# Kernel optimization log

Hardware: AMD Instinct MI355X
Metric: run time of the kernel (lower is better)

Reference implementation:

```python
import jax, jax.numpy as jnp
import numpy as np

WIDTH = 32
DEPTH = 3
B, J, K = 16, 256, 384
C_MODEL, C_OBS, C_META = 1, 1, 6
C_IN = C_MODEL + C_OBS + C_META  # concat channels fed to image_mlp


def _mlp(h, W_stack, b_stack):
    # depth x (Linear -> ReLU) hidden blocks
    for d in range(W_stack.shape[0]):
        h = jax.nn.relu(h @ W_stack[d] + b_stack[d])
    return h


def setup_inputs() -> dict:
    key = jax.random.key(0)
    ks = jax.random.split(key, 14)
    Imodel = jax.random.normal(ks[0], (B, J, K, C_MODEL), jnp.float32)
    Iobs = jax.random.normal(ks[1], (B, J, K, C_OBS), jnp.float32)
    metadata = jax.random.normal(ks[2], (B, J, K, C_META), jnp.float32)
    mask = jax.random.randint(ks[3], (B, J, K, 1), 0, 2) > 0

    def init_w(k, fan_in, fan_out):
        return jax.random.normal(k, (fan_in, fan_out), jnp.float32) / np.sqrt(fan_in)

    params = dict(
        W_img_in=init_w(ks[4], C_IN, WIDTH),
        b_img_in=jnp.zeros((WIDTH,), jnp.float32),
        W_img=jax.random.normal(ks[5], (DEPTH, WIDTH, WIDTH), jnp.float32) / np.sqrt(WIDTH),
        b_img=jnp.zeros((DEPTH, WIDTH), jnp.float32),
        W_lin_in=init_w(ks[6], C_META, WIDTH),
        b_lin_in=jnp.zeros((WIDTH,), jnp.float32),
        W_mlp=jax.random.normal(ks[7], (DEPTH, WIDTH, WIDTH), jnp.float32) / np.sqrt(WIDTH),
        b_mlp=jnp.zeros((DEPTH, WIDTH), jnp.float32),
        W_out=init_w(ks[8], WIDTH, 1),
        b_out=jnp.zeros((1,), jnp.float32),
    )
    return dict(Imodel=Imodel, Iobs=Iobs, metadata=metadata, mask=mask,
                sample_size=32, **params)


def reference(Imodel, Iobs, metadata, mask, sample_size,
              W_img_in, b_img_in, W_img, b_img,
              W_lin_in, b_lin_in, W_mlp, b_mlp, W_out, b_out):
    batch = Iobs.shape[0]
    # p: probability of each image having any observed reflection, normalized
    p = jnp.any(mask, axis=-2)[..., 0].astype(jnp.float32)  # [B, J]
    p = p / jnp.sum(p, axis=-1, keepdims=True)
    # multinomial without replacement via Gumbel top-k (fixed key)
    g = jax.random.gumbel(jax.random.key(42), p.shape, jnp.float32)
    scores = jnp.log(p) + g  # -inf where p == 0, never selected
    _, j = jax.lax.top_k(scores, sample_size)  # [B, S]
    idx = j[:, :, None, None]  # broadcast over K and channel dims

    im = jnp.take_along_axis(Imodel, idx, axis=1)    # [B, S, K, 1]
    io = jnp.take_along_axis(Iobs, idx, axis=1)      # [B, S, K, 1]
    md = jnp.take_along_axis(metadata, idx, axis=1)  # [B, S, K, 6]
    image_data = jnp.concatenate((im, io, md), axis=-1)  # [B, S, K, 8]
    image_mask = jnp.take_along_axis(mask, idx, axis=1).astype(jnp.float32)  # [B, S, K, 1]

    # image_mlp: input linear + depth hidden blocks
    h = image_data @ W_img_in + b_img_in
    h = _mlp(h, W_img, b_img)  # [B, S, K, WIDTH]
    # masked mean over sampled reflections
    image_rep = jnp.sum(image_mask * h, axis=(1, 2), keepdims=True)
    image_rep = image_rep / jnp.sum(image_mask, axis=(1, 2), keepdims=True)  # [B,1,1,WIDTH]

    scale = metadata @ W_lin_in + b_lin_in  # [B, J, K, WIDTH]
    scale = scale + image_rep
    scale = _mlp(scale, W_mlp, b_mlp)
    scale = scale @ W_out + b_out  # [B, J, K, 1]
    return jnp.where(mask, scale, 0.0)
```

## Files before the change

### kernel.cpp

```cpp
#include <hip/hip_runtime.h>
#include <hip/hip_bf16.h>
#include <stdint.h>

#define BB   16
#define JJ   256
#define KK   384
#define NROW (BB * JJ)
#define NPOS ((size_t)BB * JJ * KK)

#define WS_FLAG  0
#define WS_SEL   64
#define WS_VINT  2176
#define WS_VBYTE (WS_VINT + NROW * 4)
#define WS_PART  (WS_VBYTE + NROW * 4)
#define WS_REPB  (WS_PART + 512 * 33 * 4)

typedef float f32x4 __attribute__((ext_vector_type(4)));
typedef short bf16x8 __attribute__((ext_vector_type(8)));

__device__ __forceinline__ uint32_t rotl32(uint32_t x, int r) {
  return (x << r) | (x >> (32 - r));
}

__device__ __forceinline__ void threefry2x32_k42(uint32_t c0, uint32_t c1,
                                                 uint32_t& o0, uint32_t& o1) {
  const uint32_t ks0 = 0u, ks1 = 42u, ks2 = 0x1BD11BDAu ^ 0u ^ 42u;
  uint32_t x0 = c0 + ks0, x1 = c1 + ks1;
#define TFR(r) { x0 += x1; x1 = rotl32(x1, r); x1 ^= x0; }
  TFR(13) TFR(15) TFR(26) TFR(6)   x0 += ks1; x1 += ks2 + 1u;
  TFR(17) TFR(29) TFR(16) TFR(24)  x0 += ks2; x1 += ks0 + 2u;
  TFR(13) TFR(15) TFR(26) TFR(6)   x0 += ks0; x1 += ks1 + 3u;
  TFR(17) TFR(29) TFR(16) TFR(24)  x0 += ks1; x1 += ks2 + 4u;
  TFR(13) TFR(15) TFR(26) TFR(6)   x0 += ks2; x1 += ks0 + 5u;
#undef TFR
  o0 = x0; o1 = x1;
}

__device__ __forceinline__ uint32_t jax_bits(uint32_t t) {
  uint32_t o0, o1;
  threefry2x32_k42(0u, t, o0, o1);
  return o0 ^ o1;
}

__device__ __forceinline__ void split2(float x, short& h, short& l) {
  const unsigned short hu = __builtin_bit_cast(unsigned short, __float2bfloat16(x));
  const float hf = __builtin_bit_cast(float, (uint32_t)hu << 16);
  h = (short)hu;
  l = (short)__builtin_bit_cast(unsigned short, __float2bfloat16(x - hf));
}

__global__ __launch_bounds__(256) void k_valid(const void* __restrict__ maskp,
                                               int* __restrict__ valid_int,
                                               int* __restrict__ valid_byte) {
  const int row = blockIdx.x * 4 + (threadIdx.x >> 6);
  const int lane = threadIdx.x & 63;
  const uint32_t* wi = (const uint32_t*)maskp + (size_t)row * 384;
  int v = 0;
#pragma unroll
  for (int i = 0; i < 6; ++i) v |= (wi[lane + i * 64] != 0u);
  const unsigned long long bi = __ballot(v);
  const uint32_t* wb = (const uint32_t*)maskp + (size_t)row * 96;
  int u = 0;
  for (int i = lane; i < 96; i += 64) u |= (wb[i] != 0u);
  const unsigned long long bu = __ballot(u);
  if (lane == 0) {
    valid_int[row] = (bi != 0ull) ? 1 : 0;
    valid_byte[row] = (bu != 0ull) ? 1 : 0;
  }
}

__global__ void k_select(const void* __restrict__ maskp,
                         const int* __restrict__ valid_int,
                         const int* __restrict__ valid_byte,
                         const int* __restrict__ sample_size,
                         int* __restrict__ flag_out, int* __restrict__ sel) {
  const int b = blockIdx.x, lane = threadIdx.x;
  const uint32_t* mw = (const uint32_t*)maskp;
  int big = 0;
#pragma unroll
  for (int i = 0; i < 16; ++i) big |= (mw[lane + i * 64] > 1u);
  const int fl = (__ballot(big) != 0ull) ? 1 : 0;
  if (b == 0 && lane == 0) flag_out[0] = fl;
  const int* valid = fl ? valid_byte : valid_int;

  uint32_t comp[4];
#pragma unroll
  for (int q = 0; q < 4; ++q) {
    const int j = lane * 4 + q;
    const uint32_t ub = jax_bits((uint32_t)(b * 256 + j)) >> 9;
    const uint32_t key = valid[b * 256 + j] ? (ub + 1u) : 0u;
    comp[q] = (key << 8) | (uint32_t)(255 - j);
  }
  int S = sample_size[0];
  if (S > 32) S = 32;
  for (int s = 0; s < S; ++s) {
    uint32_t wm = comp[0];
    wm = comp[1] > wm ? comp[1] : wm;
    wm = comp[2] > wm ? comp[2] : wm;
    wm = comp[3] > wm ? comp[3] : wm;
#pragma unroll
    for (int off = 32; off; off >>= 1) {
      const uint32_t o = __shfl_xor(wm, off);
      wm = o > wm ? o : wm;
    }
    if (wm == 0u) {
      if (lane == 0) sel[b * 32 + s] = 0;
    } else {
#pragma unroll
      for (int q = 0; q < 4; ++q) {
        if (comp[q] == wm) {
          sel[b * 32 + s] = 255 - (int)(comp[q] & 0xFFu);
          comp[q] = 0u;
        }
      }
    }
  }
  for (int s2 = S + lane; s2 < 32; s2 += 64) sel[b * 32 + s2] = 0;
}

__global__ __launch_bounds__(256, 1) void k_image(
    const float* __restrict__ Imodel, const float* __restrict__ Iobs,
    const float* __restrict__ md, const void* __restrict__ maskp,
    const int* __restrict__ flag, const int* __restrict__ sel,
    const int* __restrict__ sample_size,
    const float* __restrict__ W_in, const float* __restrict__ b_in,
    const float* __restrict__ Wd, const float* __restrict__ bd,
    float* __restrict__ partial) {
  __shared__ float lds_t[4][16 * 36];
  __shared__ float red[4 * 33];
  const int tid = threadIdx.x, wid = tid >> 6, lane = tid & 63;
  const int g = lane >> 4, c = lane & 15;
  const int blk = blockIdx.x;
  const int b = blk >> 5, s = blk & 31;
  const bool active = (s < sample_size[0]);
  const int j = sel[b * 32 + s] & 255;
  const size_t pos0 = ((size_t)(b * JJ + j)) * KK + (size_t)wid * 96;
  const int fl = flag[0];

  float Win[8][8];
#pragma unroll
  for (int cc = 0; cc < 8; ++cc)
#pragma unroll
    for (int e = 0; e < 8; ++e) Win[cc][e] = W_in[cc * 32 + g * 8 + e];
  float b0v[8];
#pragma unroll
  for (int e = 0; e < 8; ++e) b0v[e] = b_in[g * 8 + e];

  bf16x8 Bh[3][2], Bl[3][2];
#pragma unroll
  for (int d = 0; d < 3; ++d)
#pragma unroll
    for (int ct = 0; ct < 2; ++ct)
#pragma unroll
      for (int e = 0; e < 8; ++e) {
        const float w = Wd[d * 1024 + (g * 8 + e) * 32 + ct * 16 + c];
        short hh, ll; split2(w, hh, ll);
        Bh[d][ct][e] = hh; Bl[d][ct][e] = ll;
      }
  float bias_v[3][2];
#pragma unroll
  for (int d = 0; d < 3; ++d) {
    bias_v[d][0] = bd[d * 32 + c];
    bias_v[d][1] = bd[d * 32 + 16 + c];
  }
  float* myl = lds_t[wid];

  float acc0 = 0.f, acc1 = 0.f, cntv = 0.f;

  for (int t = 0; t < 6; ++t) {
    const size_t tb = pos0 + (size_t)t * 16;
    const size_t p = tb + c;
    float in[8];
    in[0] = Imodel[p];
    in[1] = Iobs[p];
    const float* mp = md + p * 6;
    const float2 v0 = *(const float2*)(mp);
    const float2 v1 = *(const float2*)(mp + 2);
    const float2 v2 = *(const float2*)(mp + 4);
    in[2] = v0.x; in[3] = v0.y; in[4] = v1.x; in[5] = v1.y;
    in[6] = v2.x; in[7] = v2.y;

    bf16x8 ah, al;
#pragma unroll
    for (int e = 0; e < 8; ++e) {
      float h = b0v[e];
#pragma unroll
      for (int cc = 0; cc < 8; ++cc) h = fmaf(in[cc], Win[cc][e], h);
      short hh, ll; split2(h, hh, ll);
      ah[e] = hh; al[e] = ll;
    }

#pragma unroll
    for (int d = 0; d < 3; ++d) {
      f32x4 a0 = {0.f, 0.f, 0.f, 0.f}, a1 = {0.f, 0.f, 0.f, 0.f};
      a0 = __builtin_amdgcn_mfma_f32_16x16x32_bf16(ah, Bh[d][0], a0, 0, 0, 0);
      a0 = __builtin_amdgcn_mfma_f32_16x16x32_bf16(al, Bh[d][0], a0, 0, 0, 0);
      a0 = __builtin_amdgcn_mfma_f32_16x16x32_bf16(ah, Bl[d][0], a0, 0, 0, 0);
      a1 = __builtin_amdgcn_mfma_f32_16x16x32_bf16(ah, Bh[d][1], a1, 0, 0, 0);
      a1 = __builtin_amdgcn_mfma_f32_16x16x32_bf16(al, Bh[d][1], a1, 0, 0, 0);
      a1 = __builtin_amdgcn_mfma_f32_16x16x32_bf16(ah, Bl[d][1], a1, 0, 0, 0);
#pragma unroll
      for (int r = 0; r < 4; ++r) {
        a0[r] = fmaxf(a0[r] + bias_v[d][0], 0.f);
        a1[r] = fmaxf(a1[r] + bias_v[d][1], 0.f);
      }
      if (d < 2) {
#pragma unroll
        for (int r = 0; r < 4; ++r) {
          myl[(g * 4 + r) * 36 + c] = a0[r];
          myl[(g * 4 + r) * 36 + 16 + c] = a1[r];
        }
#pragma unroll
        for (int e = 0; e < 8; ++e) {
          const float h = myl[c * 36 + g * 8 + e];
          short hh, ll; split2(h, hh, ll);
          ah[e] = hh; al[e] = ll;
        }
      } else {
        float mr[4];
        if (fl) {
          const uint32_t mw = *(const uint32_t*)((const uint8_t*)maskp + tb + g * 4);
          mr[0] = (mw & 0x000000FFu) ? 1.f : 0.f;
          mr[1] = (mw & 0x0000FF00u) ? 1.f : 0.f;
          mr[2] = (mw & 0x00FF0000u) ? 1.f : 0.f;
          mr[3] = (mw & 0xFF000000u) ? 1.f : 0.f;
        } else {
          const int4 mi = *(const int4*)((const int*)maskp + tb + g * 4);
          mr[0] = mi.x ? 1.f : 0.f;
          mr[1] = mi.y ? 1.f : 0.f;
          mr[2] = mi.z ? 1.f : 0.f;
          mr[3] = mi.w ? 1.f : 0.f;
        }
        if (!active) { mr[0] = mr[1] = mr[2] = mr[3] = 0.f; }
#pragma unroll
        for (int r = 0; r < 4; ++r) {
          acc0 = fmaf(mr[r], a0[r], acc0);
          acc1 = fmaf(mr[r], a1[r], acc1);
          cntv += mr[r];
        }
      }
    }
  }

  acc0 += __shfl_xor(acc0, 16); acc0 += __shfl_xor(acc0, 32);
  acc1 += __shfl_xor(acc1, 16); acc1 += __shfl_xor(acc1, 32);
  cntv += __shfl_xor(cntv, 16); cntv += __shfl_xor(cntv, 32);
  if (lane < 16) {
    red[wid * 33 + lane] = acc0;
    red[wid * 33 + 16 + lane] = acc1;
  }
  if (lane == 0) red[wid * 33 + 32] = cntv;
  __syncthreads();
  if (tid < 33) {
    partial[blk * 33 + tid] =
        red[tid] + red[33 + tid] + red[66 + tid] + red[99 + tid];
  }
}

__global__ void k_rep(const float* __restrict__ partial,
                      const float* __restrict__ b_lin,
                      float* __restrict__ rep_bias) {
  const int b = blockIdx.x, n = threadIdx.x;
  float sum = 0.f, cnt = 0.f;
  for (int s = 0; s < 32; ++s) {
    sum += partial[(b * 32 + s) * 33 + n];
    cnt += partial[(b * 32 + s) * 33 + 32];
  }
  rep_bias[b * 32 + n] = b_lin[n] + sum / cnt;
}

__global__ __launch_bounds__(256, 2) void k_scale(
    const float* __restrict__ md, const void* __restrict__ maskp,
    const int* __restrict__ flag,
    const float* __restrict__ W_lin, const float* __restrict__ rep_bias,
    const float* __restrict__ Wd, const float* __restrict__ bd,
    const float* __restrict__ W_out, const float* __restrict__ b_out,
    float* __restrict__ out) {
  const int tid = threadIdx.x;
  const int wid = tid >> 6, lane = tid & 63;
  const int g = lane >> 4, c = lane & 15;
  const int job = blockIdx.x * 4 + wid;
  const int b = job / 384;
  const size_t pos0 = (size_t)job * 256;
  const int fl = flag[0];
  const bool gLt2 = (g < 2);

  bf16x8 AW[2];
#pragma unroll
  for (int ct = 0; ct < 2; ++ct) {
    const float rb = rep_bias[b * 32 + ct * 16 + c];
    short rbh, rbl; split2(rb, rbh, rbl);
#pragma unroll
    for (int e = 0; e < 8; ++e) {
      short v = 0;
      if (e < 6) {
        const float w = W_lin[e * 32 + ct * 16 + c];
        short wh, wl; split2(w, wh, wl);
        v = gLt2 ? wh : wl;
      } else if (g == 0) {
        v = (e == 6) ? rbh : rbl;
      }
      AW[ct][e] = v;
    }
  }

  bf16x8 AhW[3][2], AlW[3][2];
#pragma unroll
  for (int d = 0; d < 3; ++d)
#pragma unroll
    for (int ct = 0; ct < 2; ++ct)
#pragma unroll
      for (int e = 0; e < 8; ++e) {
        const int f = (e < 4) ? (4 * g + e) : (16 + 4 * g + (e - 4));
        const float w = Wd[d * 1024 + f * 32 + ct * 16 + c];
        short hh, ll; split2(w, hh, ll);
        AhW[d][ct][e] = hh; AlW[d][ct][e] = ll;
      }
  float bs0[3][4], bs1[3][4];
#pragma unroll
  for (int d = 0; d < 3; ++d)
#pragma unroll
    for (int r = 0; r < 4; ++r) {
      bs0[d][r] = bd[d * 32 + g * 4 + r];
      bs1[d][r] = bd[d * 32 + 16 + g * 4 + r];
    }
  float wo0[4], wo1[4];
#pragma unroll
  for (int r = 0; r < 4; ++r) {
    wo0[r] = W_out[g * 4 + r];
    wo1[r] = W_out[16 + g * 4 + r];
  }
  const float bo = b_out[0];

  float mv[6];
  uint32_t mk;
  {
    const float* mrow = md + (pos0 + c) * 6;
    const float2 a01 = *(const float2*)(mrow);
    const float2 a23 = *(const float2*)(mrow + 2);
    const float2 a45 = *(const float2*)(mrow + 4);
    mv[0] = a01.x; mv[1] = a01.y; mv[2] = a23.x;
    mv[3] = a23.y; mv[4] = a45.x; mv[5] = a45.y;
    mk = fl ? (uint32_t)((const uint8_t*)maskp)[pos0 + c]
            : ((const uint32_t*)maskp)[pos0 + c];
  }

  for (int t = 0; t < 16; ++t) {
    const size_t tb = pos0 + (size_t)t * 16;

    float mvn[6];
    uint32_t mkn = 0;
    if (t < 15) {
      const float* mrow = md + (tb + 16 + c) * 6;
      const float2 a01 = *(const float2*)(mrow);
      const float2 a23 = *(const float2*)(mrow + 2);
      const float2 a45 = *(const float2*)(mrow + 4);
      mvn[0] = a01.x; mvn[1] = a01.y; mvn[2] = a23.x;
      mvn[3] = a23.y; mvn[4] = a45.x; mvn[5] = a45.y;
      mkn = fl ? (uint32_t)((const uint8_t*)maskp)[tb + 16 + c]
               : ((const uint32_t*)maskp)[tb + 16 + c];
    }

    short xh[6], xl[6];
#pragma unroll
    for (int i = 0; i < 6; ++i) split2(mv[i], xh[i], xl[i]);
    bf16x8 Bin;
#pragma unroll
    for (int e = 0; e < 8; ++e) {
      short v;
      if (e < 6) v = (g & 1) ? xl[e] : xh[e];
      else       v = (g == 0) ? (short)0x3F80 : (short)0;
      Bin[e] = v;
    }

    const f32x4 z = {0.f, 0.f, 0.f, 0.f};
    f32x4 dT0 = __builtin_amdgcn_mfma_f32_16x16x32_bf16(AW[0], Bin, z, 0, 0, 0);
    f32x4 dT1 = __builtin_amdgcn_mfma_f32_16x16x32_bf16(AW[1], Bin, z, 0, 0, 0);

    bf16x8 Bh, Bl;
#pragma unroll
    for (int r = 0; r < 4; ++r) {
      short hh, ll;
      split2(dT0[r], hh, ll); Bh[r] = hh;     Bl[r] = ll;
      split2(dT1[r], hh, ll); Bh[4 + r] = hh; Bl[4 + r] = ll;
    }

#pragma unroll
    for (int d = 0; d < 3; ++d) {
      dT0 = __builtin_amdgcn_mfma_f32_16x16x32_bf16(AhW[d][0], Bh, z, 0, 0, 0);
      dT0 = __builtin_amdgcn_mfma_f32_16x16x32_bf16(AlW[d][0], Bh, dT0, 0, 0, 0);
      dT0 = __builtin_amdgcn_mfma_f32_16x16x32_bf16(AhW[d][0], Bl, dT0, 0, 0, 0);
      dT1 = __builtin_amdgcn_mfma_f32_16x16x32_bf16(AhW[d][1], Bh, z, 0, 0, 0);
      dT1 = __builtin_amdgcn_mfma_f32_16x16x32_bf16(AlW[d][1], Bh, dT1, 0, 0, 0);
      dT1 = __builtin_amdgcn_mfma_f32_16x16x32_bf16(AhW[d][1], Bl, dT1, 0, 0, 0);
      if (d < 2) {
#pragma unroll
        for (int r = 0; r < 4; ++r) {
          const float x0 = fmaxf(dT0[r] + bs0[d][r], 0.f);
          const float x1 = fmaxf(dT1[r] + bs1[d][r], 0.f);
          short hh, ll;
          split2(x0, hh, ll); Bh[r] = hh;     Bl[r] = ll;
          split2(x1, hh, ll); Bh[4 + r] = hh; Bl[4 + r] = ll;
        }
      } else {
        float sum = 0.f;
#pragma unroll
        for (int r = 0; r < 4; ++r) {
          const float x0 = fmaxf(dT0[r] + bs0[2][r], 0.f);
          const float x1 = fmaxf(dT1[r] + bs1[2][r], 0.f);
          sum = fmaf(x0, wo0[r], sum);
          sum = fmaf(x1, wo1[r], sum);
        }
        sum += __shfl_xor(sum, 16);
        sum += __shfl_xor(sum, 32);
        if (g == 0) out[tb + c] = mk ? (sum + bo) : 0.0f;
      }
    }

#pragma unroll
    for (int i = 0; i < 6; ++i) mv[i] = mvn[i];
    mk = mkn;
  }
}

extern "C" void kernel_launch(void* const* d_in, const int* in_sizes, int n_in,
                              void* d_out, int out_size, void* d_ws, size_t ws_size,
                              hipStream_t stream) {
  const float* Imodel   = (const float*)d_in[0];
  const float* Iobs     = (const float*)d_in[1];
  const float* metadata = (const float*)d_in[2];
  const void*  mask     = d_in[3];
  const int*   sample_size = (const int*)d_in[4];
  const float* W_img_in = (const float*)d_in[5];
  const float* b_img_in = (const float*)d_in[6];
  const float* W_img    = (const float*)d_in[7];
  const float* b_img    = (const float*)d_in[8];
  const float* W_lin_in = (const float*)d_in[9];
  const float* b_lin_in = (const float*)d_in[10];
  const float* W_mlp    = (const float*)d_in[11];
  const float* b_mlp    = (const float*)d_in[12];
  const float* W_out    = (const float*)d_in[13];
  const float* b_out    = (const float*)d_in[14];
  float* out = (float*)d_out;

  char* ws = (char*)d_ws;
  int*   flag     = (int*)(ws + WS_FLAG);
  int*   sel      = (int*)(ws + WS_SEL);
  int*   vint     = (int*)(ws + WS_VINT);
  int*   vbyte    = (int*)(ws + WS_VBYTE);
  float* partial  = (float*)(ws + WS_PART);
  float* rep_bias = (float*)(ws + WS_REPB);

  k_valid<<<NROW / 4, 256, 0, stream>>>(mask, vint, vbyte);
  k_select<<<BB, 64, 0, stream>>>(mask, vint, vbyte, sample_size, flag, sel);
  k_image<<<512, 256, 0, stream>>>(Imodel, Iobs, metadata, mask, flag, sel,
                                   sample_size, W_img_in, b_img_in, W_img,
                                   b_img, partial);
  k_rep<<<BB, 32, 0, stream>>>(partial, b_lin_in, rep_bias);
  k_scale<<<1536, 256, 0, stream>>>(metadata, mask, flag, W_lin_in, rep_bias,
                                    W_mlp, b_mlp, W_out, b_out, out);
}
```

Before: 83.99 us.

## Transpose image MLP to register-only MFMA chain and interleave two tiles in scale

Result: slower. 94.76 us (+12.8%).

```diff
diff --git a/kernel.cpp b/kernel.cpp
--- a/kernel.cpp
+++ b/kernel.cpp
@@ -17,6 +17,10 @@
 
 typedef float f32x4 __attribute__((ext_vector_type(4)));
 typedef short bf16x8 __attribute__((ext_vector_type(8)));
+
+struct FragU { union { bf16x8 v; uint32_t u[4]; }; };
+
+#define PIN(x) asm volatile("" : "+v"(x))
 
 __device__ __forceinline__ uint32_t rotl32(uint32_t x, int r) {
   return (x << r) | (x >> (32 - r));
@@ -49,6 +53,39 @@
   l = (short)__builtin_bit_cast(unsigned short, __float2bfloat16(x - hf));
 }
 
+__device__ __forceinline__ void split_pk(float x0, float x1,
+                                         uint32_t& ph, uint32_t& pl) {
+  const uint32_t h0 = (uint32_t)__builtin_bit_cast(unsigned short, __float2bfloat16(x0));
+  const uint32_t h1 = (uint32_t)__builtin_bit_cast(unsigned short, __float2bfloat16(x1));
+  ph = h0 | (h1 << 16);
+  const float f0 = __builtin_bit_cast(float, h0 << 16);
+  const float f1 = __builtin_bit_cast(float, h1 << 16);
+  const uint32_t l0 = (uint32_t)__builtin_bit_cast(unsigned short, __float2bfloat16(x0 - f0));
+  const uint32_t l1 = (uint32_t)__builtin_bit_cast(unsigned short, __float2bfloat16(x1 - f1));
+  pl = l0 | (l1 << 16);
+}
+
+__device__ __forceinline__ void refrag_ll(const f32x4 dT0, const f32x4 dT1,
+                                          bf16x8& Bh, bf16x8& Bl) {
+  FragU H, L;
+  split_pk(dT0[0], dT0[1], H.u[0], L.u[0]);
+  split_pk(dT0[2], dT0[3], H.u[1], L.u[1]);
+  split_pk(dT1[0], dT1[1], H.u[2], L.u[2]);
+  split_pk(dT1[2], dT1[3], H.u[3], L.u[3]);
+  Bh = H.v; Bl = L.v;
+}
+
+__device__ __forceinline__ void refrag_br(f32x4 dT0, f32x4 dT1,
+                                          const f32x4 b0, const f32x4 b1,
+                                          bf16x8& Bh, bf16x8& Bl) {
+#pragma unroll
+  for (int r = 0; r < 4; ++r) {
+    dT0[r] = fmaxf(dT0[r] + b0[r], 0.f);
+    dT1[r] = fmaxf(dT1[r] + b1[r], 0.f);
+  }
+  refrag_ll(dT0, dT1, Bh, Bl);
+}
+
 __global__ __launch_bounds__(256) void k_valid(const void* __restrict__ maskp,
                                                int* __restrict__ valid_int,
                                                int* __restrict__ valid_byte) {
@@ -126,7 +163,6 @@
     const float* __restrict__ W_in, const float* __restrict__ b_in,
     const float* __restrict__ Wd, const float* __restrict__ bd,
     float* __restrict__ partial) {
-  __shared__ float lds_t[4][16 * 36];
   __shared__ float red[4 * 33];
   const int tid = threadIdx.x, wid = tid >> 6, lane = tid & 63;
   const int g = lane >> 4, c = lane & 15;
@@ -137,119 +173,124 @@
   const size_t pos0 = ((size_t)(b * JJ + j)) * KK + (size_t)wid * 96;
   const int fl = flag[0];
 
-  float Win[8][8];
-#pragma unroll
-  for (int cc = 0; cc < 8; ++cc)
-#pragma unroll
-    for (int e = 0; e < 8; ++e) Win[cc][e] = W_in[cc * 32 + g * 8 + e];
-  float b0v[8];
-#pragma unroll
-  for (int e = 0; e < 8; ++e) b0v[e] = b_in[g * 8 + e];
-
-  bf16x8 Bh[3][2], Bl[3][2];
+  bf16x8 AWi[2];
+#pragma unroll
+  for (int ct = 0; ct < 2; ++ct) {
+    short bh, bl; split2(b_in[ct * 16 + c], bh, bl);
+#pragma unroll
+    for (int e = 0; e < 8; ++e) {
+      short v;
+      if (g <= 1) {
+        short hh, ll; split2(W_in[e * 32 + ct * 16 + c], hh, ll);
+        v = hh;
+      } else if (g == 2) {
+        short hh, ll; split2(W_in[e * 32 + ct * 16 + c], hh, ll);
+        v = ll;
+      } else {
+        v = (e == 0) ? bh : ((e == 1) ? bl : (short)0);
+      }
+      AWi[ct][e] = v;
+    }
+  }
+
+  bf16x8 AhW[3][2], AlW[3][2];
 #pragma unroll
   for (int d = 0; d < 3; ++d)
 #pragma unroll
     for (int ct = 0; ct < 2; ++ct)
 #pragma unroll
       for (int e = 0; e < 8; ++e) {
-        const float w = Wd[d * 1024 + (g * 8 + e) * 32 + ct * 16 + c];
-        short hh, ll; split2(w, hh, ll);
-        Bh[d][ct][e] = hh; Bl[d][ct][e] = ll;
-      }
-  float bias_v[3][2];
-#pragma unroll
-  for (int d = 0; d < 3; ++d) {
-    bias_v[d][0] = bd[d * 32 + c];
-    bias_v[d][1] = bd[d * 32 + 16 + c];
-  }
-  float* myl = lds_t[wid];
-
-  float acc0 = 0.f, acc1 = 0.f, cntv = 0.f;
+        const int f = (e < 4) ? (4 * g + e) : (16 + 4 * g + (e - 4));
+        short hh, ll; split2(Wd[d * 1024 + f * 32 + ct * 16 + c], hh, ll);
+        AhW[d][ct][e] = hh; AlW[d][ct][e] = ll;
+      }
+  f32x4 bsA[3], bsB[3];
+#pragma unroll
+  for (int d = 0; d < 3; ++d)
+#pragma unroll
+    for (int r = 0; r < 4; ++r) {
+      bsA[d][r] = bd[d * 32 + 4 * g + r];
+      bsB[d][r] = bd[d * 32 + 16 + 4 * g + r];
+    }
+
+  f32x4 acc0 = {0.f, 0.f, 0.f, 0.f}, acc1 = {0.f, 0.f, 0.f, 0.f};
+  float cntv = 0.f;
+  const f32x4 z = {0.f, 0.f, 0.f, 0.f};
 
   for (int t = 0; t < 6; ++t) {
+    PIN(AWi[0]); PIN(AWi[1]);
+#pragma unroll
+    for (int d = 0; d < 3; ++d) {
+      PIN(AhW[d][0]); PIN(AhW[d][1]); PIN(AlW[d][0]); PIN(AlW[d][1]);
+    }
     const size_t tb = pos0 + (size_t)t * 16;
     const size_t p = tb + c;
-    float in[8];
-    in[0] = Imodel[p];
-    in[1] = Iobs[p];
+    const float i0 = Imodel[p];
+    const float i1 = Iobs[p];
     const float* mp = md + p * 6;
     const float2 v0 = *(const float2*)(mp);
     const float2 v1 = *(const float2*)(mp + 2);
     const float2 v2 = *(const float2*)(mp + 4);
-    in[2] = v0.x; in[3] = v0.y; in[4] = v1.x; in[5] = v1.y;
-    in[6] = v2.x; in[7] = v2.y;
-
-    bf16x8 ah, al;
-#pragma unroll
-    for (int e = 0; e < 8; ++e) {
-      float h = b0v[e];
-#pragma unroll
-      for (int cc = 0; cc < 8; ++cc) h = fmaf(in[cc], Win[cc][e], h);
-      short hh, ll; split2(h, hh, ll);
-      ah[e] = hh; al[e] = ll;
-    }
+    float m;
+    if (fl) m = (((const uint8_t*)maskp)[p] != 0) ? 1.f : 0.f;
+    else    m = (((const int*)maskp)[p] != 0) ? 1.f : 0.f;
+    if (!active) m = 0.f;
+
+    uint32_t ph[4], pl[4];
+    split_pk(i0, i1, ph[0], pl[0]);
+    split_pk(v0.x, v0.y, ph[1], pl[1]);
+    split_pk(v1.x, v1.y, ph[2], pl[2]);
+    split_pk(v2.x, v2.y, ph[3], pl[3]);
+    FragU Bi;
+#pragma unroll
+    for (int i = 0; i < 4; ++i) {
+      const uint32_t t0 = (g == 1) ? pl[i] : ph[i];
+      Bi.u[i] = (g == 3) ? ((i == 0) ? 0x3F803F80u : 0u) : t0;
+    }
+
+    f32x4 dT0 = __builtin_amdgcn_mfma_f32_16x16x32_bf16(AWi[0], Bi.v, z, 0, 0, 0);
+    f32x4 dT1 = __builtin_amdgcn_mfma_f32_16x16x32_bf16(AWi[1], Bi.v, z, 0, 0, 0);
+    bf16x8 Bh, Bl;
+    refrag_ll(dT0, dT1, Bh, Bl);
 
 #pragma unroll
     for (int d = 0; d < 3; ++d) {
-      f32x4 a0 = {0.f, 0.f, 0.f, 0.f}, a1 = {0.f, 0.f, 0.f, 0.f};
-      a0 = __builtin_amdgcn_mfma_f32_16x16x32_bf16(ah, Bh[d][0], a0, 0, 0, 0);
-      a0 = __builtin_amdgcn_mfma_f32_16x16x32_bf16(al, Bh[d][0], a0, 0, 0, 0);
-      a0 = __builtin_amdgcn_mfma_f32_16x16x32_bf16(ah, Bl[d][0], a0, 0, 0, 0);
-      a1 = __builtin_amdgcn_mfma_f32_16x16x32_bf16(ah, Bh[d][1], a1, 0, 0, 0);
-      a1 = __builtin_amdgcn_mfma_f32_16x16x32_bf16(al, Bh[d][1], a1, 0, 0, 0);
-      a1 = __builtin_amdgcn_mfma_f32_16x16x32_bf16(ah, Bl[d][1], a1, 0, 0, 0);
-#pragma unroll
-      for (int r = 0; r < 4; ++r) {
-        a0[r] = fmaxf(a0[r] + bias_v[d][0], 0.f);
-        a1[r] = fmaxf(a1[r] + bias_v[d][1], 0.f);
-      }
+      dT0 = __builtin_amdgcn_mfma_f32_16x16x32_bf16(AhW[d][0], Bh, z, 0, 0, 0);
+      dT1 = __builtin_amdgcn_mfma_f32_16x16x32_bf16(AhW[d][1], Bh, z, 0, 0, 0);
+      dT0 = __builtin_amdgcn_mfma_f32_16x16x32_bf16(AlW[d][0], Bh, dT0, 0, 0, 0);
+      dT1 = __builtin_amdgcn_mfma_f32_16x16x32_bf16(AlW[d][1], Bh, dT1, 0, 0, 0);
+      dT0 = __builtin_amdgcn_mfma_f32_16x16x32_bf16(AhW[d][0], Bl, dT0, 0, 0, 0);
+      dT1 = __builtin_amdgcn_mfma_f32_16x16x32_bf16(AhW[d][1], Bl, dT1, 0, 0, 0);
       if (d < 2) {
+        refrag_br(dT0, dT1, bsA[d], bsB[d], Bh, Bl);
+      } else {
 #pragma unroll
         for (int r = 0; r < 4; ++r) {
-          myl[(g * 4 + r) * 36 + c] = a0[r];
-          myl[(g * 4 + r) * 36 + 16 + c] = a1[r];
+          acc0[r] = fmaf(m, fmaxf(dT0[r] + bsA[2][r], 0.f), acc0[r]);
+          acc1[r] = fmaf(m, fmaxf(dT1[r] + bsB[2][r], 0.f), acc1[r]);
         }
-#pragma unroll
-        for (int e = 0; e < 8; ++e) {
-          const float h = myl[c * 36 + g * 8 + e];
-          short hh, ll; split2(h, hh, ll);
-          ah[e] = hh; al[e] = ll;
-        }
-      } else {
-        float mr[4];
-        if (fl) {
-          const uint32_t mw = *(const uint32_t*)((const uint8_t*)maskp + tb + g * 4);
-          mr[0] = (mw & 0x000000FFu) ? 1.f : 0.f;
-          mr[1] = (mw & 0x0000FF00u) ? 1.f : 0.f;
-          mr[2] = (mw & 0x00FF0000u) ? 1.f : 0.f;
-          mr[3] = (mw & 0xFF000000u) ? 1.f : 0.f;
-        } else {
-          const int4 mi = *(const int4*)((const int*)maskp + tb + g * 4);
-          mr[0] = mi.x ? 1.f : 0.f;
-          mr[1] = mi.y ? 1.f : 0.f;
-          mr[2] = mi.z ? 1.f : 0.f;
-          mr[3] = mi.w ? 1.f : 0.f;
-        }
-        if (!active) { mr[0] = mr[1] = mr[2] = mr[3] = 0.f; }
-#pragma unroll
-        for (int r = 0; r < 4; ++r) {
-          acc0 = fmaf(mr[r], a0[r], acc0);
-          acc1 = fmaf(mr[r], a1[r], acc1);
-          cntv += mr[r];
-        }
-      }
-    }
-  }
-
-  acc0 += __shfl_xor(acc0, 16); acc0 += __shfl_xor(acc0, 32);
-  acc1 += __shfl_xor(acc1, 16); acc1 += __shfl_xor(acc1, 32);
-  cntv += __shfl_xor(cntv, 16); cntv += __shfl_xor(cntv, 32);
-  if (lane < 16) {
-    red[wid * 33 + lane] = acc0;
-    red[wid * 33 + 16 + lane] = acc1;
-  }
-  if (lane == 0) red[wid * 33 + 32] = cntv;
+        cntv += m;
+      }
+    }
+  }
+
+#pragma unroll
+  for (int off = 1; off < 16; off <<= 1) {
+#pragma unroll
+    for (int r = 0; r < 4; ++r) {
+      acc0[r] += __shfl_xor(acc0[r], off);
+      acc1[r] += __shfl_xor(acc1[r], off);
+    }
+    cntv += __shfl_xor(cntv, off);
+  }
+  if (c == 0) {
+#pragma unroll
+    for (int r = 0; r < 4; ++r) {
+      red[wid * 33 + 4 * g + r] = acc0[r];
+      red[wid * 33 + 16 + 4 * g + r] = acc1[r];
+    }
+    if (g == 0) red[wid * 33 + 32] = cntv;
+  }
   __syncthreads();
   if (tid < 33) {
     partial[blk * 33 + tid] =
@@ -269,7 +310,7 @@
   rep_bias[b * 32 + n] = b_lin[n] + sum / cnt;
 }
 
-__global__ __launch_bounds__(256, 2) void k_scale(
+__global__ __launch_bounds__(256, 1) void k_scale(
     const float* __restrict__ md, const void* __restrict__ maskp,
     const int* __restrict__ flag,
     const float* __restrict__ W_lin, const float* __restrict__ rep_bias,
@@ -288,14 +329,12 @@
   bf16x8 AW[2];
 #pragma unroll
   for (int ct = 0; ct < 2; ++ct) {
-    const float rb = rep_bias[b * 32 + ct * 16 + c];
-    short rbh, rbl; split2(rb, rbh, rbl);
+    short rbh, rbl; split2(rep_bias[b * 32 + ct * 16 + c], rbh, rbl);
 #pragma unroll
     for (int e = 0; e < 8; ++e) {
       short v = 0;
       if (e < 6) {
-        const float w = W_lin[e * 32 + ct * 16 + c];
-        short wh, wl; split2(w, wh, wl);
+        short wh, wl; split2(W_lin[e * 32 + ct * 16 + c], wh, wl);
         v = gLt2 ? wh : wl;
       } else if (g == 0) {
         v = (e == 6) ? rbh : rbl;
@@ -312,114 +351,156 @@
 #pragma unroll
       for (int e = 0; e < 8; ++e) {
         const int f = (e < 4) ? (4 * g + e) : (16 + 4 * g + (e - 4));
-        const float w = Wd[d * 1024 + f * 32 + ct * 16 + c];
-        short hh, ll; split2(w, hh, ll);
+        short hh, ll; split2(Wd[d * 1024 + f * 32 + ct * 16 + c], hh, ll);
         AhW[d][ct][e] = hh; AlW[d][ct][e] = ll;
       }
-  float bs0[3][4], bs1[3][4];
+  f32x4 bsA[3], bsB[3];
 #pragma unroll
   for (int d = 0; d < 3; ++d)
 #pragma unroll
     for (int r = 0; r < 4; ++r) {
-      bs0[d][r] = bd[d * 32 + g * 4 + r];
-      bs1[d][r] = bd[d * 32 + 16 + g * 4 + r];
-    }
-  float wo0[4], wo1[4];
+      bsA[d][r] = bd[d * 32 + 4 * g + r];
+      bsB[d][r] = bd[d * 32 + 16 + 4 * g + r];
+    }
+  f32x4 woA, woB;
 #pragma unroll
   for (int r = 0; r < 4; ++r) {
-    wo0[r] = W_out[g * 4 + r];
-    wo1[r] = W_out[16 + g * 4 + r];
+    woA[r] = W_out[4 * g + r];
+    woB[r] = W_out[16 + 4 * g + r];
   }
   const float bo = b_out[0];
-
-  float mv[6];
-  uint32_t mk;
+  const uint32_t bias_word = (g == 0) ? 0x00003F80u : 0u;
+
+  float mvA[6], mvB[6];
+  uint32_t mkA, mkB;
   {
-    const float* mrow = md + (pos0 + c) * 6;
-    const float2 a01 = *(const float2*)(mrow);
-    const float2 a23 = *(const float2*)(mrow + 2);
-    const float2 a45 = *(const float2*)(mrow + 4);
-    mv[0] = a01.x; mv[1] = a01.y; mv[2] = a23.x;
-    mv[3] = a23.y; mv[4] = a45.x; mv[5] = a45.y;
-    mk = fl ? (uint32_t)((const uint8_t*)maskp)[pos0 + c]
-            : ((const uint32_t*)maskp)[pos0 + c];
-  }
-
-  for (int t = 0; t < 16; ++t) {
-    const size_t tb = pos0 + (size_t)t * 16;
-
-    float mvn[6];
-    uint32_t mkn = 0;
-    if (t < 15) {
-      const float* mrow = md + (tb + 16 + c) * 6;
-      const float2 a01 = *(const float2*)(mrow);
-      const float2 a23 = *(const float2*)(mrow + 2);
-      const float2 a45 = *(const float2*)(mrow + 4);
-      mvn[0] = a01.x; mvn[1] = a01.y; mvn[2] = a23.x;
-      mvn[3] = a23.y; mvn[4] = a45.x; mvn[5] = a45.y;
-      mkn = fl ? (uint32_t)((const uint8_t*)maskp)[tb + 16 + c]
-               : ((const uint32_t*)maskp)[tb + 16 + c];
-    }
-
-    short xh[6], xl[6];
-#pragma unroll
-    for (int i = 0; i < 6; ++i) split2(mv[i], xh[i], xl[i]);
-    bf16x8 Bin;
-#pragma unroll
-    for (int e = 0; e < 8; ++e) {
-      short v;
-      if (e < 6) v = (g & 1) ? xl[e] : xh[e];
-      else       v = (g == 0) ? (short)0x3F80 : (short)0;
-      Bin[e] = v;
-    }
-
-    const f32x4 z = {0.f, 0.f, 0.f, 0.f};
-    f32x4 dT0 = __builtin_amdgcn_mfma_f32_16x16x32_bf16(AW[0], Bin, z, 0, 0, 0);
-    f32x4 dT1 = __builtin_amdgcn_mfma_f32_16x16x32_bf16(AW[1], Bin, z, 0, 0, 0);
-
-    bf16x8 Bh, Bl;
-#pragma unroll
-    for (int r = 0; r < 4; ++r) {
-      short hh, ll;
-      split2(dT0[r], hh, ll); Bh[r] = hh;     Bl[r] = ll;
-      split2(dT1[r], hh, ll); Bh[4 + r] = hh; Bl[4 + r] = ll;
-    }
-
+    const float* ra = md + (pos0 + c) * 6;
+    const float2 a01 = *(const float2*)(ra);
+    const float2 a23 = *(const float2*)(ra + 2);
+    const float2 a45 = *(const float2*)(ra + 4);
+    mvA[0] = a01.x; mvA[1] = a01.y; mvA[2] = a23.x;
+    mvA[3] = a23.y; mvA[4] = a45.x; mvA[5] = a45.y;
+    const float* rb2 = md + (pos0 + 16 + c) * 6;
+    const float2 b01 = *(const float2*)(rb2);
+    const float2 b23 = *(const float2*)(rb2 + 2);
+    const float2 b45 = *(const float2*)(rb2 + 4);
+    mvB[0] = b01.x; mvB[1] = b01.y; mvB[2] = b23.x;
+    mvB[3] = b23.y; mvB[4] = b45.x; mvB[5] = b45.y;
+    if (fl) {
+      mkA = (uint32_t)((const uint8_t*)maskp)[pos0 + c];
+      mkB = (uint32_t)((const uint8_t*)maskp)[pos0 + 16 + c];
+    } else {
+      mkA = ((const uint32_t*)maskp)[pos0 + c];
+      mkB = ((const uint32_t*)maskp)[pos0 + 16 + c];
+    }
+  }
+
+  const f32x4 z = {0.f, 0.f, 0.f, 0.f};
+
+  for (int tp = 0; tp < 8; ++tp) {
+    PIN(AW[0]); PIN(AW[1]);
 #pragma unroll
     for (int d = 0; d < 3; ++d) {
-      dT0 = __builtin_amdgcn_mfma_f32_16x16x32_bf16(AhW[d][0], Bh, z, 0, 0, 0);
-      dT0 = __builtin_amdgcn_mfma_f32_16x16x32_bf16(AlW[d][0], Bh, dT0, 0, 0, 0);
-      dT0 = __builtin_amdgcn_mfma_f32_16x16x32_bf16(AhW[d][0], Bl, dT0, 0, 0, 0);
-      dT1 = __builtin_amdgcn_mfma_f32_16x16x32_bf16(AhW[d][1], Bh, z, 0, 0, 0);
-      dT1 = __builtin_amdgcn_mfma_f32_16x16x32_bf16(AlW[d][1], Bh, dT1, 0, 0, 0);
-      dT1 = __builtin_amdgcn_mfma_f32_16x16x32_bf16(AhW[d][1], Bl, dT1, 0, 0, 0);
+      PIN(AhW[d][0]); PIN(AhW[d][1]); PIN(AlW[d][0]); PIN(AlW[d][1]);
+      PIN(bsA[d]); PIN(bsB[d]);
+    }
+    PIN(woA); PIN(woB);
+
+    const size_t tbA = pos0 + (size_t)tp * 32;
+    const size_t tbB = tbA + 16;
+
+    float nvA[6] = {0, 0, 0, 0, 0, 0}, nvB[6] = {0, 0, 0, 0, 0, 0};
+    uint32_t nkA = 0, nkB = 0;
+    if (tp < 7) {
+      const float* ra = md + (tbA + 32 + c) * 6;
+      const float2 a01 = *(const float2*)(ra);
+      const float2 a23 = *(const float2*)(ra + 2);
+      const float2 a45 = *(const float2*)(ra + 4);
+      nvA[0] = a01.x; nvA[1] = a01.y; nvA[2] = a23.x;
+      nvA[3] = a23.y; nvA[4] = a45.x; nvA[5] = a45.y;
+      const float* rb2 = md + (tbA + 48 + c) * 6;
+      const float2 b01 = *(const float2*)(rb2);
+      const float2 b23 = *(const float2*)(rb2 + 2);
+      const float2 b45 = *(const float2*)(rb2 + 4);
+      nvB[0] = b01.x; nvB[1] = b01.y; nvB[2] = b23.x;
+      nvB[3] = b23.y; nvB[4] = b45.x; nvB[5] = b45.y;
+      if (fl) {
+        nkA = (uint32_t)((const uint8_t*)maskp)[tbA + 32 + c];
+        nkB = (uint32_t)((const uint8_t*)maskp)[tbA + 48 + c];
+      } else {
+        nkA = ((const uint32_t*)maskp)[tbA + 32 + c];
+        nkB = ((const uint32_t*)maskp)[tbA + 48 + c];
+      }
+    }
+
+    FragU BinA, BinB;
+    {
+      uint32_t ph0, pl0, ph1, pl1, ph2, pl2;
+      split_pk(mvA[0], mvA[1], ph0, pl0);
+      split_pk(mvA[2], mvA[3], ph1, pl1);
+      split_pk(mvA[4], mvA[5], ph2, pl2);
+      BinA.u[0] = (g & 1) ? pl0 : ph0;
+      BinA.u[1] = (g & 1) ? pl1 : ph1;
+      BinA.u[2] = (g & 1) ? pl2 : ph2;
+      BinA.u[3] = bias_word;
+      split_pk(mvB[0], mvB[1], ph0, pl0);
+      split_pk(mvB[2], mvB[3], ph1, pl1);
+      split_pk(mvB[4], mvB[5], ph2, pl2);
+      BinB.u[0] = (g & 1) ? pl0 : ph0;
+      BinB.u[1] = (g & 1) ? pl1 : ph1;
+      BinB.u[2] = (g & 1) ? pl2 : ph2;
+      BinB.u[3] = bias_word;
+    }
+
+    f32x4 dT0A = __builtin_amdgcn_mfma_f32_16x16x32_bf16(AW[0], BinA.v, z, 0, 0, 0);
+    f32x4 dT0B = __builtin_amdgcn_mfma_f32_16x16x32_bf16(AW[0], BinB.v, z, 0, 0, 0);
+    f32x4 dT1A = __builtin_amdgcn_mfma_f32_16x16x32_bf16(AW[1], BinA.v, z, 0, 0, 0);
+    f32x4 dT1B = __builtin_amdgcn_mfma_f32_16x16x32_bf16(AW[1], BinB.v, z, 0, 0, 0);
+
+    bf16x8 BhA, BlA, BhB, BlB;
+    refrag_ll(dT0A, dT1A, BhA, BlA);
+    refrag_ll(dT0B, dT1B, BhB, BlB);
+
+#pragma unroll
+    for (int d = 0; d < 3; ++d) {
+      dT0A = __builtin_amdgcn_mfma_f32_16x16x32_bf16(AhW[d][0], BhA, z, 0, 0, 0);
+      dT0B = __builtin_amdgcn_mfma_f32_16x16x32_bf16(AhW[d][0], BhB, z, 0, 0, 0);
+      dT1A = __builtin_amdgcn_mfma_f32_16x16x32_bf16(AhW[d][1], BhA, z, 0, 0, 0);
+      dT1B = __builtin_amdgcn_mfma_f32_16x16x32_bf16(AhW[d][1], BhB, z, 0, 0, 0);
+      dT0A = __builtin_amdgcn_mfma_f32_16x16x32_bf16(AlW[d][0], BhA, dT0A, 0, 0, 0);
+      dT0B = __builtin_amdgcn_mfma_f32_16x16x32_bf16(AlW[d][0], BhB, dT0B, 0, 0, 0);
+      dT1A = __builtin_amdgcn_mfma_f32_16x16x32_bf16(AlW[d][1], BhA, dT1A, 0, 0, 0);
+      dT1B = __builtin_amdgcn_mfma_f32_16x16x32_bf16(AlW[d][1], BhB, dT1B, 0, 0, 0);
+      dT0A = __builtin_amdgcn_mfma_f32_16x16x32_bf16(AhW[d][0], BlA, dT0A, 0, 0, 0);
+      dT0B = __builtin_amdgcn_mfma_f32_16x16x32_bf16(AhW[d][0], BlB, dT0B, 0, 0, 0);
+      dT1A = __builtin_amdgcn_mfma_f32_16x16x32_bf16(AhW[d][1], BlA, dT1A, 0, 0, 0);
+      dT1B = __builtin_amdgcn_mfma_f32_16x16x32_bf16(AhW[d][1], BlB, dT1B, 0, 0, 0);
       if (d < 2) {
+        refrag_br(dT0A, dT1A, bsA[d], bsB[d], BhA, BlA);
+        refrag_br(dT0B, dT1B, bsA[d], bsB[d], BhB, BlB);
+      } else {
+        float sumA = 0.f, sumB = 0.f;
 #pragma unroll
         for (int r = 0; r < 4; ++r) {
-          const float x0 = fmaxf(dT0[r] + bs0[d][r], 0.f);
-          const float x1 = fmaxf(dT1[r] + bs1[d][r], 0.f);
-          short hh, ll;
-          split2(x0, hh, ll); Bh[r] = hh;     Bl[r] = ll;
-          split2(x1, hh, ll); Bh[4 + r] = hh; Bl[4 + r] = ll;
+          sumA = fmaf(fmaxf(dT0A[r] + bsA[2][r], 0.f), woA[r], sumA);
+          sumA = fmaf(fmaxf(dT1A[r] + bsB[2][r], 0.f), woB[r], sumA);
+          sumB = fmaf(fmaxf(dT0B[r] + bsA[2][r], 0.f), woA[r], sumB);
+          sumB = fmaf(fmaxf(dT1B[r] + bsB[2][r], 0.f), woB[r], sumB);
         }
-      } else {
-        float sum = 0.f;
-#pragma unroll
-        for (int r = 0; r < 4; ++r) {
-          const float x0 = fmaxf(dT0[r] + bs0[2][r], 0.f);
-          const float x1 = fmaxf(dT1[r] + bs1[2][r], 0.f);
-          sum = fmaf(x0, wo0[r], sum);
-          sum = fmaf(x1, wo1[r], sum);
+        sumA += __shfl_xor(sumA, 16);
+        sumA += __shfl_xor(sumA, 32);
+        sumB += __shfl_xor(sumB, 16);
+        sumB += __shfl_xor(sumB, 32);
+        if (g == 0) {
+          out[tbA + c] = mkA ? (sumA + bo) : 0.0f;
+          out[tbB + c] = mkB ? (sumB + bo) : 0.0f;
         }
-        sum += __shfl_xor(sum, 16);
-        sum += __shfl_xor(sum, 32);
-        if (g == 0) out[tb + c] = mk ? (sum + bo) : 0.0f;
-      }
-    }
-
-#pragma unroll
-    for (int i = 0; i < 6; ++i) mv[i] = mvn[i];
-    mk = mkn;
+      }
+    }
+
+#pragma unroll
+    for (int i = 0; i < 6; ++i) { mvA[i] = nvA[i]; mvB[i] = nvB[i]; }
+    mkA = nkA; mkB = nkB;
   }
 }
 
```
